# Performance work log

Hardware: AMD Instinct MI355X
Metric: run time of the kernel (lower is better)

The kernel has to match this reference:

```python
import jax, jax.numpy as jnp
import numpy as np

TW = 25; HID = 128; LAYERS = 6; SPATIAL = 1; NVAR = 1
TMAX = 4.0; TMIN = 0.0; RES_T = 250.0; DOM = 16.0
N = 65536; B = 8; E = 393216
EPS = 1e-5


def swish(x):
    return x * jax.nn.sigmoid(x)


def _forward(u, x_pos, t_pos, variables,
             emb_w1, emb_b1, emb_w2, emb_b2,
             m1_w, m1_b, m2_w, m2_b,
             u1_w, u1_b, u2_w, u2_b,
             c1_w, c1_b, c2_w, c2_b,
             edge_index, batch):
    t_norm = t_pos / TMAX                       # [N]
    pos = x_pos / DOM                           # [N, 1] normalized by domain extent
    node_in = jnp.concatenate([u, pos, t_norm[:, None], variables], axis=-1)
    f = swish(node_in @ emb_w1 + emb_b1)
    f = swish(f @ emb_w2 + emb_b2)              # [N, HID]

    var_all = jnp.concatenate([t_norm[:, None], variables], axis=-1)  # [N, NVAR+1]
    src, dst = edge_index[0], edge_index[1]     # PyG: x_j = x[src], x_i = x[dst]
    du = u[dst] - u[src]                        # [E, TW]
    dp = pos[dst] - pos[src]                    # [E, SPATIAL]
    v_i = var_all[dst]                          # [E, NVAR+1]

    ones_e = jnp.ones((E,), f.dtype)
    deg = jnp.maximum(jax.ops.segment_sum(ones_e, dst, num_segments=N), 1.0)
    ones_n = jnp.ones((N,), f.dtype)
    gcount = jnp.maximum(jax.ops.segment_sum(ones_n, batch, num_segments=B), 1.0)

    for l in range(LAYERS):
        # message: concat(x_i, x_j, u_i-u_j, pos_i-pos_j, vars_i) -> 2-layer MLP
        m = jnp.concatenate([f[dst], f[src], du, dp, v_i], axis=-1)  # [E, 284]
        m = swish(m @ m1_w[l] + m1_b[l])
        m = swish(m @ m2_w[l] + m2_b[l])
        agg = jax.ops.segment_sum(m, dst, num_segments=N) / deg[:, None]  # mean aggr
        # update: concat(x, message, vars) -> 2-layer MLP, residual (in==out)
        h = jnp.concatenate([f, agg, var_all], axis=-1)  # [N, 258]
        h = swish(h @ u1_w[l] + u1_b[l])
        h = swish(h @ u2_w[l] + u2_b[l])
        h = f + h
        # InstanceNorm over nodes within each graph, per feature (no affine)
        mean = jax.ops.segment_sum(h, batch, num_segments=B) / gcount[:, None]
        var = jax.ops.segment_sum(h * h, batch, num_segments=B) / gcount[:, None] - mean * mean
        f = (h - mean[batch]) * jax.lax.rsqrt(var[batch] + EPS)

    # output CNN head over feature axis: [N, 1, HID] -> [N, 1, TW]
    y = jax.lax.conv_general_dilated(f[:, None, :], c1_w, (3,), 'VALID',
                                     dimension_numbers=('NCH', 'OIH', 'NCH'))
    y = swish(y + c1_b[None, :, None])
    y = jax.lax.conv_general_dilated(y, c2_w, (1,), 'VALID',
                                     dimension_numbers=('NCH', 'OIH', 'NCH'))
    diff = y[:, 0, :] + c2_b[0]                 # [N, TW]

    dt = jnp.cumsum(jnp.full((TW,), (TMAX - TMIN) / RES_T, dtype=f.dtype))
    out = u[:, -1][:, None] + dt[None, :] * diff
    return out


def setup_inputs() -> dict:
    key = jax.random.key(0)
    keys = iter(jax.random.split(key, 128))

    def lin(i, o):
        s = 1.0 / np.sqrt(i)
        w = jax.random.uniform(next(keys), (i, o), jnp.float32, -s, s)
        b = jax.random.uniform(next(keys), (o,), jnp.float32, -s, s)
        return w, b

    def stacked(i, o):
        ws, bs = zip(*[lin(i, o) for _ in range(LAYERS)])
        return jnp.stack(ws), jnp.stack(bs)

    def conv(o, i, k):
        s = 1.0 / np.sqrt(i * k)
        w = jax.random.uniform(next(keys), (o, i, k), jnp.float32, -s, s)
        b = jax.random.uniform(next(keys), (o,), jnp.float32, -s, s)
        return w, b

    emb_w1, emb_b1 = lin(TW + SPATIAL + 1 + NVAR, HID)
    emb_w2, emb_b2 = lin(HID, HID)
    m1_w, m1_b = stacked(2 * HID + TW + SPATIAL + NVAR + 1, HID)
    m2_w, m2_b = stacked(HID, HID)
    u1_w, u1_b = stacked(2 * HID + NVAR + 1, HID)
    u2_w, u2_b = stacked(HID, HID)
    c1_w, c1_b = conv(8, 1, 16)
    c2_w, c2_b = conv(1, 8, 14)

    u = jax.random.normal(next(keys), (N, TW), jnp.float32)
    x_pos = jax.random.uniform(next(keys), (N, SPATIAL), jnp.float32) * DOM
    t_pos = jax.random.uniform(next(keys), (N,), jnp.float32) * TMAX
    variables = jax.random.normal(next(keys), (N, NVAR), jnp.float32)
    edge_index = jax.random.randint(next(keys), (2, E), 0, N, jnp.int32)
    batch = jnp.sort(jax.random.randint(next(keys), (N,), 0, B, jnp.int32))

    return {'u': u, 'x_pos': x_pos, 't_pos': t_pos, 'variables': variables,
            'edge_index': edge_index, 'batch': batch,
            'emb_w1': emb_w1, 'emb_b1': emb_b1, 'emb_w2': emb_w2, 'emb_b2': emb_b2,
            'm1_w': m1_w, 'm1_b': m1_b, 'm2_w': m2_w, 'm2_b': m2_b,
            'u1_w': u1_w, 'u1_b': u1_b, 'u2_w': u2_w, 'u2_b': u2_b,
            'c1_w': c1_w, 'c1_b': c1_b, 'c2_w': c2_w, 'c2_b': c2_b}


def reference(u, x_pos, t_pos, variables, edge_index, batch,
              emb_w1, emb_b1, emb_w2, emb_b2,
              m1_w, m1_b, m2_w, m2_b,
              u1_w, u1_b, u2_w, u2_b,
              c1_w, c1_b, c2_w, c2_b):
    return _forward(u, x_pos, t_pos, variables,
                    emb_w1, emb_b1, emb_w2, emb_b2,
                    m1_w, m1_b, m2_w, m2_b,
                    u1_w, u1_b, u2_w, u2_b,
                    c1_w, c1_b, c2_w, c2_b,
                    edge_index, batch)
```

## Files before the change

### kernel.cpp

```cpp
#include <hip/hip_runtime.h>
#include <hip/hip_bf16.h>

#define N_NODES 65536
#define N_EDGES 393216
#define NB 8
#define HID 128
#define TW 25
#define LAYERS 6
#define BGRAPH 8
#define EPSF 1e-5f
#define TILE_E 128

typedef __attribute__((ext_vector_type(8))) short bf16x8;
typedef __attribute__((ext_vector_type(4))) float f32x4;

__device__ __forceinline__ float swishf(float x) {
    float den = 1.0f + __expf(-x);
    float r;
    asm("v_rcp_f32 %0, %1" : "=v"(r) : "v"(den));
    return x * r;
}

__device__ __forceinline__ unsigned short f2bf(float x) {
    unsigned int u = __float_as_uint(x);
    u += 0x7fffu + ((u >> 16) & 1u);
    return (unsigned short)(u >> 16);
}

__device__ __forceinline__ unsigned int cvtpk2bf(float lo, float hi) {
    unsigned int r;
    asm("v_cvt_pk_bf16_f32 %0, %1, %2" : "=v"(r) : "v"(lo), "v"(hi));
    return r;
}

__device__ __forceinline__ unsigned short f2bf_rne(float x) {
    unsigned int r;
    asm("v_cvt_pk_bf16_f32 %0, %1, %2" : "=v"(r) : "v"(x), "v"(x));
    return (unsigned short)r;
}

__device__ __forceinline__ float bf2f(unsigned short v) {
    return __uint_as_float(((unsigned int)v) << 16);
}

__global__ void gcount_kernel(const int* __restrict__ batch, float* __restrict__ gcount) {
    int b = threadIdx.x;
    if (b >= BGRAPH) return;
    auto lb = [&](int key) {
        int lo = 0, hi = N_NODES;
        while (lo < hi) { int mid = (lo + hi) >> 1; if (batch[mid] < key) lo = mid + 1; else hi = mid; }
        return lo;
    };
    int c = lb(b + 1) - lb(b);
    gcount[b] = c > 0 ? (float)c : 1.0f;
}

__global__ void count_kernel(const int* __restrict__ ei, int* __restrict__ cnt) {
    int e = blockIdx.x * 256 + threadIdx.x;
    if (e < N_EDGES) atomicAdd(&cnt[ei[N_EDGES + e]], 1);
}

__global__ __launch_bounds__(256) void block_sum_kernel(const int* __restrict__ cnt, int* __restrict__ bsum) {
    __shared__ int s[256];
    int t = threadIdx.x;
    s[t] = cnt[blockIdx.x * 256 + t];
    __syncthreads();
    for (int st = 128; st > 0; st >>= 1) {
        if (t < st) s[t] += s[t + st];
        __syncthreads();
    }
    if (t == 0) bsum[blockIdx.x] = s[0];
}

__global__ __launch_bounds__(256) void scan_bsum_kernel(const int* __restrict__ bsum, int* __restrict__ bpref) {
    __shared__ int s[256];
    int t = threadIdx.x;
    int orig = bsum[t];
    s[t] = orig;
    __syncthreads();
    for (int st = 1; st < 256; st <<= 1) {
        int v = (t >= st) ? s[t - st] : 0;
        __syncthreads();
        s[t] += v;
        __syncthreads();
    }
    bpref[t] = s[t] - orig;
}

__global__ __launch_bounds__(256) void offsets_kernel(const int* __restrict__ cnt, const int* __restrict__ bpref,
                                                      int* __restrict__ cursor) {
    __shared__ int s[256];
    int t = threadIdx.x;
    int base = blockIdx.x * 256;
    int orig = cnt[base + t];
    s[t] = orig;
    __syncthreads();
    for (int st = 1; st < 256; st <<= 1) {
        int v = (t >= st) ? s[t - st] : 0;
        __syncthreads();
        s[t] += v;
        __syncthreads();
    }
    cursor[base + t] = s[t] - orig + bpref[blockIdx.x];
}

__global__ void scatter_kernel(const int* __restrict__ ei, int* __restrict__ cursor,
                               int* __restrict__ src_s, int* __restrict__ dst_s) {
    int e = blockIdx.x * 256 + threadIdx.x;
    if (e >= N_EDGES) return;
    int d = ei[N_EDGES + e];
    int pos = atomicAdd(&cursor[d], 1);
    src_s[pos] = ei[e];
    dst_s[pos] = d;
}

__global__ void w2bf_kernel(const float* __restrict__ m2_w, unsigned short* __restrict__ W2T) {
    int idx = blockIdx.x * 256 + threadIdx.x;
    int l = idx >> 14;
    int rem = idx & 16383;
    int n = rem >> 7, k = rem & 127;
    W2T[idx] = f2bf(m2_w[l * 16384 + k * HID + n]);
}

__global__ void w1t_kernel(const float* __restrict__ m1_w, unsigned short* __restrict__ wAB) {
    int idx = blockIdx.x * 256 + threadIdx.x;
    int l = idx / (2 * 128 * 160);
    int rem = idx % (2 * 128 * 160);
    int pass = rem / (128 * 160);
    int o = (rem % (128 * 160)) / 160;
    int k = rem % 160;
    const float* M = m1_w + (size_t)l * 284 * 128;
    float v;
    if (k < 128) {
        v = M[(pass ? 128 + k : k) * 128 + o];
    } else {
        int ku = k - 128;
        if (ku < 25) v = M[(256 + ku) * 128 + o];
        else if (ku == 25) v = M[281 * 128 + o];
        else if (ku == 26) v = M[282 * 128 + o];
        else if (ku == 27) v = M[283 * 128 + o];
        else v = 0.0f;
        if (pass) v = (ku <= 25) ? -v : 0.0f;
    }
    wAB[idx] = f2bf(v);
}

__global__ void u1t_kernel(const float* __restrict__ u1_w, unsigned short* __restrict__ U1T) {
    int idx = blockIdx.x * 256 + threadIdx.x;
    int l = idx >> 15;
    int o = (idx >> 8) & 127;
    int k = idx & 255;
    U1T[idx] = f2bf(u1_w[(size_t)l * 258 * 128 + k * 128 + o]);
}

__global__ void u2t_kernel(const float* __restrict__ u2_w, unsigned short* __restrict__ U2T) {
    int idx = blockIdx.x * 256 + threadIdx.x;
    int l = idx >> 14;
    int o = (idx >> 7) & 127;
    int k = idx & 127;
    U2T[idx] = f2bf(u2_w[(size_t)l * 16384 + k * 128 + o]);
}

__global__ void wemb_kernel(const float* __restrict__ ew1, const float* __restrict__ ew2,
                            unsigned short* __restrict__ we1T, unsigned short* __restrict__ we2T) {
    int idx = blockIdx.x * 256 + threadIdx.x;
    if (idx < 4096) {
        int o = idx >> 5, k = idx & 31;
        we1T[idx] = f2bf(k < 28 ? ew1[k * HID + o] : 0.0f);
    } else {
        int j = idx - 4096;
        int o = j >> 7, k = j & 127;
        we2T[j] = f2bf(ew2[k * HID + o]);
    }
}

__global__ void xin_kernel(const float* __restrict__ u, const float* __restrict__ xpos,
                           const float* __restrict__ tpos, const float* __restrict__ vars,
                           unsigned short* __restrict__ xin) {
    int idx = blockIdx.x * 256 + threadIdx.x;
    int n = idx >> 5, k = idx & 31;
    float v;
    if (k < 25) v = u[n * TW + k];
    else if (k == 25) v = xpos[n] * (1.0f / 16.0f);
    else if (k == 26) v = tpos[n] * 0.25f;
    else if (k == 27) v = vars[n];
    else v = 0.0f;
    xin[idx] = f2bf(v);
}

__device__ __forceinline__ void abv_chunk(
    const bf16x8 (&afr)[2][5], int nb, int lr, int lk, int colbase,
    const unsigned short* __restrict__ Wp, const float* __restrict__ b1,
    unsigned short* __restrict__ Op)
{
    f32x4 acc[2][2];
    #pragma unroll
    for (int rt = 0; rt < 2; ++rt)
        #pragma unroll
        for (int cf2 = 0; cf2 < 2; ++cf2)
            acc[rt][cf2] = (f32x4){0.0f, 0.0f, 0.0f, 0.0f};
    #pragma unroll
    for (int cf2 = 0; cf2 < 2; ++cf2) {
        const unsigned short* wrow = Wp + (colbase + cf2 * 16 + lr) * 160 + lk * 8;
        #pragma unroll
        for (int ks = 0; ks < 5; ++ks) {
            bf16x8 bfr = *reinterpret_cast<const bf16x8*>(wrow + ks * 32);
            acc[0][cf2] = __builtin_amdgcn_mfma_f32_16x16x32_bf16(afr[0][ks], bfr, acc[0][cf2], 0, 0, 0);
            acc[1][cf2] = __builtin_amdgcn_mfma_f32_16x16x32_bf16(afr[1][ks], bfr, acc[1][cf2], 0, 0, 0);
        }
    }
    #pragma unroll
    for (int cf2 = 0; cf2 < 2; ++cf2) {
        int col = colbase + cf2 * 16 + lr;
        float bb = b1 ? b1[col] : 0.0f;
        #pragma unroll
        for (int rt = 0; rt < 2; ++rt) {
            #pragma unroll
            for (int j = 0; j < 4; ++j) {
                int row = nb + rt * 16 + lk * 4 + j;
                Op[(size_t)row * HID + col] = f2bf_rne(acc[rt][cf2][j] + bb);
            }
        }
    }
}

__global__ __launch_bounds__(256) void emb_abv_kernel(
    const unsigned short* __restrict__ xin_bf,
    const unsigned short* __restrict__ we1T, const float* __restrict__ eb1,
    const unsigned short* __restrict__ we2T, const float* __restrict__ eb2,
    const unsigned short* __restrict__ wA, const unsigned short* __restrict__ wB,
    const float* __restrict__ b1,
    unsigned short* __restrict__ f_bf,
    unsigned short* __restrict__ A_bf, unsigned short* __restrict__ Bv_bf)
{
    __shared__ unsigned short q_lds[4 * 32 * HID];
    const int tid = threadIdx.x;
    const int w = tid >> 6, l = tid & 63;
    const int lr = l & 15, lk = l >> 4;
    const int nb = blockIdx.x * 128 + w * 32;
    char* qbase = reinterpret_cast<char*>(q_lds) + w * 8192;

    bf16x8 xfr[2];
    #pragma unroll
    for (int rt = 0; rt < 2; ++rt)
        xfr[rt] = *reinterpret_cast<const bf16x8*>(xin_bf + (size_t)(nb + rt * 16 + lr) * 32 + lk * 8);

    #pragma unroll 1
    for (int cc = 0; cc < 4; ++cc) {
        f32x4 acc1[2][2];
        #pragma unroll
        for (int rt = 0; rt < 2; ++rt)
            #pragma unroll
            for (int cf2 = 0; cf2 < 2; ++cf2)
                acc1[rt][cf2] = (f32x4){0.0f, 0.0f, 0.0f, 0.0f};
        #pragma unroll
        for (int cf2 = 0; cf2 < 2; ++cf2) {
            bf16x8 bfr = *reinterpret_cast<const bf16x8*>(we1T + ((cc * 2 + cf2) * 16 + lr) * 32 + lk * 8);
            acc1[0][cf2] = __builtin_amdgcn_mfma_f32_16x16x32_bf16(xfr[0], bfr, acc1[0][cf2], 0, 0, 0);
            acc1[1][cf2] = __builtin_amdgcn_mfma_f32_16x16x32_bf16(xfr[1], bfr, acc1[1][cf2], 0, 0, 0);
        }
        #pragma unroll
        for (int cf2 = 0; cf2 < 2; ++cf2) {
            int col = (cc * 2 + cf2) * 16 + lr;
            float bb = eb1[col];
            #pragma unroll
            for (int rt = 0; rt < 2; ++rt)
                #pragma unroll
                for (int j = 0; j < 4; ++j) {
                    float qv = swishf(acc1[rt][cf2][j] + bb);
                    int rloc = rt * 16 + lk * 4 + j;
                    *reinterpret_cast<unsigned short*>(qbase + rloc * 256 + ((col * 2) ^ ((rloc & 7) << 4))) = f2bf_rne(qv);
                }
        }
    }

    __shared__ unsigned short f_lds2[4 * 32 * HID];
    char* fbase = reinterpret_cast<char*>(f_lds2) + w * 8192;
    #pragma unroll 1
    for (int cc = 0; cc < 4; ++cc) {
        f32x4 acc2[2][2];
        #pragma unroll
        for (int rt = 0; rt < 2; ++rt)
            #pragma unroll
            for (int cf2 = 0; cf2 < 2; ++cf2)
                acc2[rt][cf2] = (f32x4){0.0f, 0.0f, 0.0f, 0.0f};
        #pragma unroll
        for (int ks = 0; ks < 4; ++ks) {
            bf16x8 afrq[2];
            #pragma unroll
            for (int rt = 0; rt < 2; ++rt) {
                int rloc = rt * 16 + lr;
                afrq[rt] = *reinterpret_cast<const bf16x8*>(qbase + rloc * 256 + ((ks * 64 + lk * 16) ^ ((rloc & 7) << 4)));
            }
            #pragma unroll
            for (int cf2 = 0; cf2 < 2; ++cf2) {
                bf16x8 bfr = *reinterpret_cast<const bf16x8*>(we2T + ((cc * 2 + cf2) * 16 + lr) * HID + ks * 32 + lk * 8);
                acc2[0][cf2] = __builtin_amdgcn_mfma_f32_16x16x32_bf16(afrq[0], bfr, acc2[0][cf2], 0, 0, 0);
                acc2[1][cf2] = __builtin_amdgcn_mfma_f32_16x16x32_bf16(afrq[1], bfr, acc2[1][cf2], 0, 0, 0);
            }
        }
        #pragma unroll
        for (int cf2 = 0; cf2 < 2; ++cf2) {
            int col = (cc * 2 + cf2) * 16 + lr;
            float bb = eb2[col];
            #pragma unroll
            for (int rt = 0; rt < 2; ++rt)
                #pragma unroll
                for (int j = 0; j < 4; ++j) {
                    float fv = swishf(acc2[rt][cf2][j] + bb);
                    unsigned short fb = f2bf_rne(fv);
                    int rloc = rt * 16 + lk * 4 + j;
                    f_bf[(size_t)(nb + rloc) * HID + col] = fb;
                    *reinterpret_cast<unsigned short*>(fbase + rloc * 256 + ((col * 2) ^ ((rloc & 7) << 4))) = fb;
                }
        }
    }

    bf16x8 afr[2][5];
    #pragma unroll
    for (int rt = 0; rt < 2; ++rt) {
        int rloc = rt * 16 + lr;
        #pragma unroll
        for (int ks = 0; ks < 4; ++ks)
            afr[rt][ks] = *reinterpret_cast<const bf16x8*>(fbase + rloc * 256 + ((ks * 64 + lk * 16) ^ ((rloc & 7) << 4)));
        afr[rt][4] = xfr[rt];
    }
    #pragma unroll 1
    for (int cc = 0; cc < 4; ++cc) abv_chunk(afr, nb, lr, lk, cc * 32, wA, b1, A_bf);
    #pragma unroll 1
    for (int cc = 0; cc < 4; ++cc) abv_chunk(afr, nb, lr, lk, cc * 32, wB, nullptr, Bv_bf);
}

__global__ __launch_bounds__(256) void norm_abv_kernel(
    const unsigned short* __restrict__ h, const int* __restrict__ batch,
    const float* __restrict__ dsum, const float* __restrict__ dsq,
    const float* __restrict__ gcount,
    const unsigned short* __restrict__ xin_bf,
    const unsigned short* __restrict__ wA, const unsigned short* __restrict__ wB,
    const float* __restrict__ b1,
    unsigned short* __restrict__ f_bf,
    unsigned short* __restrict__ A_bf, unsigned short* __restrict__ Bv_bf)
{
    __shared__ unsigned short f_lds[32 * HID];
    const int tid = threadIdx.x;
    const int w = tid >> 6, l = tid & 63;
    const int lr = l & 15, lk = l >> 4;
    const int nb = blockIdx.x * 32;

    {
        const int ks = w;
        const int c0 = ks * 32 + lk * 8;
        #pragma unroll
        for (int rt = 0; rt < 2; ++rt) {
            int row = nb + rt * 16 + lr;
            int b = batch[row];
            float inv = 1.0f / gcount[b];
            uint4 hv4 = *reinterpret_cast<const uint4*>(h + (size_t)row * HID + c0);
            unsigned int hw[4] = {hv4.x, hv4.y, hv4.z, hv4.w};
            float4 s0 = *reinterpret_cast<const float4*>(dsum + b * HID + c0);
            float4 s1 = *reinterpret_cast<const float4*>(dsum + b * HID + c0 + 4);
            float4 q0 = *reinterpret_cast<const float4*>(dsq + b * HID + c0);
            float4 q1 = *reinterpret_cast<const float4*>(dsq + b * HID + c0 + 4);
            float o[8];
            #pragma unroll
            for (int i = 0; i < 8; ++i) {
                float hx = (i & 1) ? __uint_as_float(hw[i >> 1] & 0xffff0000u)
                                   : __uint_as_float(hw[i >> 1] << 16);
                float sm = (i < 4) ? reinterpret_cast<const float*>(&s0)[i] : reinterpret_cast<const float*>(&s1)[i - 4];
                float sq = (i < 4) ? reinterpret_cast<const float*>(&q0)[i] : reinterpret_cast<const float*>(&q1)[i - 4];
                float mean = sm * inv;
                float var = sq * inv - mean * mean;
                o[i] = (hx - mean) * rsqrtf(var + EPSF);
            }
            uint4 t;
            t.x = cvtpk2bf(o[0], o[1]);
            t.y = cvtpk2bf(o[2], o[3]);
            t.z = cvtpk2bf(o[4], o[5]);
            t.w = cvtpk2bf(o[6], o[7]);
            *reinterpret_cast<uint4*>(f_bf + (size_t)row * HID + c0) = t;
            int rloc = rt * 16 + lr;
            *reinterpret_cast<uint4*>(reinterpret_cast<char*>(f_lds) + rloc * 256 + ((c0 * 2) ^ ((rloc & 7) << 4))) = t;
        }
    }
    __syncthreads();

    bf16x8 afr[2][5];
    #pragma unroll
    for (int rt = 0; rt < 2; ++rt) {
        int rloc = rt * 16 + lr;
        #pragma unroll
        for (int ks = 0; ks < 4; ++ks)
            afr[rt][ks] = *reinterpret_cast<const bf16x8*>(
                reinterpret_cast<const char*>(f_lds) + rloc * 256 + ((ks * 64 + lk * 16) ^ ((rloc & 7) << 4)));
        afr[rt][4] = *reinterpret_cast<const bf16x8*>(xin_bf + (size_t)(nb + rt * 16 + lr) * 32 + lk * 8);
    }
    abv_chunk(afr, nb, lr, lk, w * 32, wA, b1, A_bf);
    abv_chunk(afr, nb, lr, lk, w * 32, wB, nullptr, Bv_bf);
}

__global__ __launch_bounds__(256) void edge_mfma_kernel(
    const int* __restrict__ src_s, const int* __restrict__ dst_s,
    const unsigned short* __restrict__ A_bf, const unsigned short* __restrict__ Bv_bf,
    const unsigned short* __restrict__ W2T, const float* __restrict__ b2,
    float* __restrict__ agg)
{
    const int tid = threadIdx.x;
    const int w = tid >> 6, l = tid & 63;
    const int lr = l & 15, lk = l >> 4;
    const int e0 = blockIdx.x * TILE_E + w * 32;

    bf16x8 afr[2][4];
    #pragma unroll
    for (int rt = 0; rt < 2; ++rt) {
        int e = e0 + ((lr >> 2) << 3) + rt * 4 + (lr & 3);
        int dn = dst_s[e], sn = src_s[e];
        const unsigned short* ap = A_bf + (size_t)dn * HID + lk * 8;
        const unsigned short* bp = Bv_bf + (size_t)sn * HID + lk * 8;
        #pragma unroll
        for (int ks = 0; ks < 4; ++ks) {
            uint4 av = *reinterpret_cast<const uint4*>(ap + ks * 32);
            uint4 bv = *reinterpret_cast<const uint4*>(bp + ks * 32);
            auto proc = [](unsigned int aw, unsigned int bw) -> unsigned int {
                float a0 = __uint_as_float(aw << 16), a1 = __uint_as_float(aw & 0xffff0000u);
                float b0 = __uint_as_float(bw << 16), b1 = __uint_as_float(bw & 0xffff0000u);
                return cvtpk2bf(swishf(a0 + b0), swishf(a1 + b1));
            };
            union { bf16x8 v; unsigned int u[4]; } t;
            t.u[0] = proc(av.x, bv.x);
            t.u[1] = proc(av.y, bv.y);
            t.u[2] = proc(av.z, bv.z);
            t.u[3] = proc(av.w, bv.w);
            afr[rt][ks] = t.v;
        }
    }

    const int ebase = e0 + lk * 8;
    int4 dA4 = *reinterpret_cast<const int4*>(dst_s + ebase);
    int4 dB4 = *reinterpret_cast<const int4*>(dst_s + ebase + 4);
    int d[8] = {dA4.x, dA4.y, dA4.z, dA4.w, dB4.x, dB4.y, dB4.z, dB4.w};
    bool sm[7];
    int roff[8];
    #pragma unroll
    for (int m = 0; m < 7; ++m) sm[m] = (d[m + 1] == d[m]);
    #pragma unroll
    for (int m = 0; m < 8; ++m) roff[m] = d[m] * HID;

    #pragma unroll 1
    for (int cc = 0; cc < 4; ++cc) {
        f32x4 acc[2][2];
        #pragma unroll
        for (int rt = 0; rt < 2; ++rt)
            #pragma unroll
            for (int cf2 = 0; cf2 < 2; ++cf2)
                acc[rt][cf2] = (f32x4){0.0f, 0.0f, 0.0f, 0.0f};
        #pragma unroll
        for (int cf2 = 0; cf2 < 2; ++cf2) {
            const unsigned short* wrow = W2T + ((cc * 2 + cf2) * 16 + lr) * HID + lk * 8;
            #pragma unroll
            for (int ks = 0; ks < 4; ++ks) {
                bf16x8 bfr = *reinterpret_cast<const bf16x8*>(wrow + ks * 32);
                acc[0][cf2] = __builtin_amdgcn_mfma_f32_16x16x32_bf16(afr[0][ks], bfr, acc[0][cf2], 0, 0, 0);
                acc[1][cf2] = __builtin_amdgcn_mfma_f32_16x16x32_bf16(afr[1][ks], bfr, acc[1][cf2], 0, 0, 0);
            }
        }
        #pragma unroll
        for (int cf2 = 0; cf2 < 2; ++cf2) {
            int col = (cc * 2 + cf2) * 16 + lr;
            float bias = b2[col];
            float v[8];
            #pragma unroll
            for (int m = 0; m < 8; ++m) v[m] = swishf(acc[m >> 2][cf2][m & 3] + bias);
            float run = v[0];
            #pragma unroll
            for (int m = 1; m < 8; ++m) {
                if (sm[m - 1]) run += v[m];
                else { atomicAdd(&agg[(size_t)roff[m - 1] + col], run); run = v[m]; }
            }
            atomicAdd(&agg[(size_t)roff[7] + col], run);
        }
    }
}

__global__ __launch_bounds__(256) void update_mfma_kernel(
    const unsigned short* __restrict__ f_bf, const float* __restrict__ agg,
    const int* __restrict__ cnt,
    const float* __restrict__ tpos, const float* __restrict__ vars,
    const int* __restrict__ batch,
    const unsigned short* __restrict__ U1T, const float* __restrict__ u1tv,
    const float* __restrict__ b1, const unsigned short* __restrict__ U2T,
    const float* __restrict__ b2, unsigned short* __restrict__ h,
    float* __restrict__ dsum, float* __restrict__ dsq)
{
    __shared__ unsigned short q_lds[32 * HID];
    const int tid = threadIdx.x;
    const int w = tid >> 6, l = tid & 63;
    const int lr = l & 15, lk = l >> 4;
    const int nb = blockIdx.x * 32;

    float invd[2];
    #pragma unroll
    for (int rt = 0; rt < 2; ++rt) {
        int c = cnt[nb + rt * 16 + lr];
        invd[rt] = 1.0f / (float)(c > 0 ? c : 1);
    }
    float tn[2][4], vn[2][4];
    #pragma unroll
    for (int rt = 0; rt < 2; ++rt)
        #pragma unroll
        for (int j = 0; j < 4; ++j) {
            int row = nb + rt * 16 + lk * 4 + j;
            tn[rt][j] = tpos[row] * 0.25f;
            vn[rt][j] = vars[row];
        }

    {
        f32x4 acc[2][2];
        #pragma unroll
        for (int rt = 0; rt < 2; ++rt)
            #pragma unroll
            for (int cf2 = 0; cf2 < 2; ++cf2)
                acc[rt][cf2] = (f32x4){0.0f, 0.0f, 0.0f, 0.0f};
        #pragma unroll
        for (int ks = 0; ks < 8; ++ks) {
            bf16x8 afr[2];
            #pragma unroll
            for (int rt = 0; rt < 2; ++rt) {
                int row = nb + rt * 16 + lr;
                if (ks < 4) {
                    afr[rt] = *reinterpret_cast<const bf16x8*>(f_bf + (size_t)row * HID + ks * 32 + lk * 8);
                } else {
                    const float* ap = agg + (size_t)row * HID + (ks - 4) * 32 + lk * 8;
                    float4 a0 = *reinterpret_cast<const float4*>(ap);
                    float4 a1 = *reinterpret_cast<const float4*>(ap + 4);
                    float iv = invd[rt];
                    union { bf16x8 v; unsigned int u[4]; } t;
                    t.u[0] = cvtpk2bf(a0.x * iv, a0.y * iv);
                    t.u[1] = cvtpk2bf(a0.z * iv, a0.w * iv);
                    t.u[2] = cvtpk2bf(a1.x * iv, a1.y * iv);
                    t.u[3] = cvtpk2bf(a1.z * iv, a1.w * iv);
                    afr[rt] = t.v;
                }
            }
            #pragma unroll
            for (int cf2 = 0; cf2 < 2; ++cf2) {
                bf16x8 bfr = *reinterpret_cast<const bf16x8*>(U1T + ((w * 2 + cf2) * 16 + lr) * 256 + ks * 32 + lk * 8);
                acc[0][cf2] = __builtin_amdgcn_mfma_f32_16x16x32_bf16(afr[0], bfr, acc[0][cf2], 0, 0, 0);
                acc[1][cf2] = __builtin_amdgcn_mfma_f32_16x16x32_bf16(afr[1], bfr, acc[1][cf2], 0, 0, 0);
            }
        }
        #pragma unroll
        for (int cf2 = 0; cf2 < 2; ++cf2) {
            int col = w * 32 + cf2 * 16 + lr;
            float bb = b1[col], wt = u1tv[col], wv = u1tv[HID + col];
            #pragma unroll
            for (int rt = 0; rt < 2; ++rt)
                #pragma unroll
                for (int j = 0; j < 4; ++j) {
                    float qv = swishf(acc[rt][cf2][j] + bb + tn[rt][j] * wt + vn[rt][j] * wv);
                    int rloc = rt * 16 + lk * 4 + j;
                    *reinterpret_cast<unsigned short*>(reinterpret_cast<char*>(q_lds) + rloc * 256 + ((col * 2) ^ ((rloc & 7) << 4))) = f2bf_rne(qv);
                }
        }
    }
    __syncthreads();

    const int bfirst = batch[nb];
    const bool uni = (bfirst == batch[nb + 31]);
    {
        f32x4 acc2[2][2];
        #pragma unroll
        for (int rt = 0; rt < 2; ++rt)
            #pragma unroll
            for (int cf2 = 0; cf2 < 2; ++cf2)
                acc2[rt][cf2] = (f32x4){0.0f, 0.0f, 0.0f, 0.0f};
        #pragma unroll
        for (int ks = 0; ks < 4; ++ks) {
            bf16x8 afr[2];
            #pragma unroll
            for (int rt = 0; rt < 2; ++rt) {
                int rloc = rt * 16 + lr;
                afr[rt] = *reinterpret_cast<const bf16x8*>(
                    reinterpret_cast<const char*>(q_lds) + rloc * 256 + ((ks * 64 + lk * 16) ^ ((rloc & 7) << 4)));
            }
            #pragma unroll
            for (int cf2 = 0; cf2 < 2; ++cf2) {
                bf16x8 bfr = *reinterpret_cast<const bf16x8*>(U2T + ((w * 2 + cf2) * 16 + lr) * HID + ks * 32 + lk * 8);
                acc2[0][cf2] = __builtin_amdgcn_mfma_f32_16x16x32_bf16(afr[0], bfr, acc2[0][cf2], 0, 0, 0);
                acc2[1][cf2] = __builtin_amdgcn_mfma_f32_16x16x32_bf16(afr[1], bfr, acc2[1][cf2], 0, 0, 0);
            }
        }
        #pragma unroll
        for (int cf2 = 0; cf2 < 2; ++cf2) {
            int col = w * 32 + cf2 * 16 + lr;
            float bb = b2[col];
            float s = 0.0f, s2 = 0.0f;
            #pragma unroll
            for (int rt = 0; rt < 2; ++rt)
                #pragma unroll
                for (int j = 0; j < 4; ++j) {
                    int row = nb + rt * 16 + lk * 4 + j;
                    float fres = bf2f(f_bf[(size_t)row * HID + col]);
                    float hv = fres + swishf(acc2[rt][cf2][j] + bb);
                    unsigned short hb = f2bf_rne(hv);
                    h[(size_t)row * HID + col] = hb;
                    float hvr = bf2f(hb);
                    if (uni) { s += hvr; s2 += hvr * hvr; }
                    else {
                        int b = batch[row];
                        atomicAdd(&dsum[b * HID + col], hvr);
                        atomicAdd(&dsq[b * HID + col], hvr * hvr);
                    }
                }
            if (uni) {
                s += __shfl_xor(s, 16); s += __shfl_xor(s, 32);
                s2 += __shfl_xor(s2, 16); s2 += __shfl_xor(s2, 32);
                if (lk == 0) {
                    atomicAdd(&dsum[bfirst * HID + col], s);
                    atomicAdd(&dsq[bfirst * HID + col], s2);
                }
            }
        }
    }
}

__global__ __launch_bounds__(256) void head_kernel(
    const unsigned short* __restrict__ h, const int* __restrict__ batch,
    const float* __restrict__ dsum, const float* __restrict__ dsq,
    const float* __restrict__ gcount,
    const float* __restrict__ u,
    const float* __restrict__ c1w, const float* __restrict__ c1b,
    const float* __restrict__ c2w, const float* __restrict__ c2b,
    float* __restrict__ out)
{
    __shared__ float fs[16][HID];
    __shared__ float y1[16][8][40];
    const int tid = threadIdx.x;
    const int n0 = blockIdx.x * 16;
    {
        int node = tid >> 4, cb = tid & 15;
        int n = n0 + node;
        int b = batch[n];
        float inv = 1.0f / gcount[b];
        int c0 = cb * 8;
        uint4 v = *reinterpret_cast<const uint4*>(h + (size_t)n * HID + c0);
        unsigned int wv[4] = {v.x, v.y, v.z, v.w};
        #pragma unroll
        for (int i = 0; i < 8; ++i) {
            float hx = (i & 1) ? __uint_as_float(wv[i >> 1] & 0xffff0000u)
                               : __uint_as_float(wv[i >> 1] << 16);
            float mean = dsum[b * HID + c0 + i] * inv;
            float var = dsq[b * HID + c0 + i] * inv - mean * mean;
            fs[node][c0 + i] = (hx - mean) * rsqrtf(var + EPSF);
        }
    }
    __syncthreads();
    {
        const int node = tid >> 4;
        const int rem = tid & 15;
        const int o = rem >> 1;
        const int ph = rem & 1;
        const float cb = c1b[o];
        float wk[16];
        #pragma unroll
        for (int k = 0; k < 16; ++k) wk[k] = c1w[o * 16 + k];
        for (int p = ph * 19; p < ph * 19 + 19; ++p) {
            float acc = cb;
            #pragma unroll
            for (int k = 0; k < 16; ++k) acc += fs[node][p * 3 + k] * wk[k];
            y1[node][o][p] = swishf(acc);
        }
    }
    __syncthreads();
    const float cb2 = c2b[0];
    #pragma unroll
    for (int pass = 0; pass < 2; ++pass) {
        int unit = tid + pass * 256;
        if (unit < 16 * TW) {
            int node = unit / TW, t = unit % TW;
            float acc = cb2;
            #pragma unroll
            for (int o = 0; o < 8; ++o)
                #pragma unroll
                for (int k = 0; k < 14; ++k)
                    acc += y1[node][o][t + k] * c2w[o * 14 + k];
            int n = n0 + node;
            out[n * TW + t] = u[n * TW + (TW - 1)] + (0.016f * (float)(t + 1)) * acc;
        }
    }
}

extern "C" void kernel_launch(void* const* d_in, const int* in_sizes, int n_in,
                              void* d_out, int out_size, void* d_ws, size_t ws_size,
                              hipStream_t stream)
{
    (void)in_sizes; (void)n_in; (void)out_size; (void)ws_size;
    const float* u      = (const float*)d_in[0];
    const float* xpos   = (const float*)d_in[1];
    const float* tpos   = (const float*)d_in[2];
    const float* vars   = (const float*)d_in[3];
    const int*   ei     = (const int*)d_in[4];
    const int*   batch  = (const int*)d_in[5];
    const float* emb_w1 = (const float*)d_in[6];
    const float* emb_b1 = (const float*)d_in[7];
    const float* emb_w2 = (const float*)d_in[8];
    const float* emb_b2 = (const float*)d_in[9];
    const float* m1_w   = (const float*)d_in[10];
    const float* m1_b   = (const float*)d_in[11];
    const float* m2_w   = (const float*)d_in[12];
    const float* m2_b   = (const float*)d_in[13];
    const float* u1_w   = (const float*)d_in[14];
    const float* u1_b   = (const float*)d_in[15];
    const float* u2_w   = (const float*)d_in[16];
    const float* u2_b   = (const float*)d_in[17];
    const float* c1w    = (const float*)d_in[18];
    const float* c1b    = (const float*)d_in[19];
    const float* c2w    = (const float*)d_in[20];
    const float* c2b    = (const float*)d_in[21];
    float* out = (float*)d_out;

    char* ws = (char*)d_ws;
    const size_t fbytes = (size_t)N_NODES * HID * sizeof(float);
    float* agg    = (float*)(ws);
    char*  p      = ws + fbytes;
    unsigned short* h_bf   = (unsigned short*)p;  p += (size_t)N_NODES * HID * 2;
    unsigned short* A_bf   = (unsigned short*)p;  p += (size_t)N_NODES * HID * 2;
    unsigned short* Bv_bf  = (unsigned short*)p;  p += (size_t)N_NODES * HID * 2;
    unsigned short* f_bf   = (unsigned short*)p;  p += (size_t)N_NODES * HID * 2;
    unsigned short* xin_bf = (unsigned short*)p;  p += (size_t)N_NODES * 32 * 2;
    int* cnt      = (int*)p;               p += (size_t)N_NODES * 4;
    int* cursor   = (int*)p;               p += (size_t)N_NODES * 4;
    int* src_s    = (int*)p;               p += (size_t)N_EDGES * 4;
    int* dst_s    = (int*)p;               p += (size_t)N_EDGES * 4;
    int* bsum     = (int*)p;               p += 256 * 4;
    int* bpref    = (int*)p;               p += 256 * 4;
    float* dsumL  = (float*)p;             p += (size_t)LAYERS * BGRAPH * HID * 4;
    float* dsqL   = (float*)p;             p += (size_t)LAYERS * BGRAPH * HID * 4;
    float* gcount = (float*)p;             p += BGRAPH * 4;
    unsigned short* W2T  = (unsigned short*)p;  p += (size_t)LAYERS * HID * HID * 2;
    unsigned short* wAB  = (unsigned short*)p;  p += (size_t)LAYERS * 2 * 128 * 160 * 2;
    unsigned short* U1T  = (unsigned short*)p;  p += (size_t)LAYERS * 128 * 256 * 2;
    unsigned short* U2T  = (unsigned short*)p;  p += (size_t)LAYERS * 128 * 128 * 2;
    unsigned short* we1T = (unsigned short*)p;  p += 128 * 32 * 2;
    unsigned short* we2T = (unsigned short*)p;  p += 128 * 128 * 2;

    hipMemsetAsync(cnt, 0, (size_t)N_NODES * 4, stream);
    count_kernel<<<N_EDGES / 256, 256, 0, stream>>>(ei, cnt);
    block_sum_kernel<<<N_NODES / 256, 256, 0, stream>>>(cnt, bsum);
    scan_bsum_kernel<<<1, 256, 0, stream>>>(bsum, bpref);
    offsets_kernel<<<N_NODES / 256, 256, 0, stream>>>(cnt, bpref, cursor);
    scatter_kernel<<<N_EDGES / 256, 256, 0, stream>>>(ei, cursor, src_s, dst_s);

    w2bf_kernel<<<LAYERS * HID * HID / 256, 256, 0, stream>>>(m2_w, W2T);
    w1t_kernel<<<LAYERS * 2 * 128 * 160 / 256, 256, 0, stream>>>(m1_w, wAB);
    u1t_kernel<<<LAYERS * 128 * 256 / 256, 256, 0, stream>>>(u1_w, U1T);
    u2t_kernel<<<LAYERS * 128 * 128 / 256, 256, 0, stream>>>(u2_w, U2T);
    wemb_kernel<<<80, 256, 0, stream>>>(emb_w1, emb_w2, we1T, we2T);
    xin_kernel<<<N_NODES * 32 / 256, 256, 0, stream>>>(u, xpos, tpos, vars, xin_bf);
    gcount_kernel<<<1, 64, 0, stream>>>(batch, gcount);
    hipMemsetAsync(dsumL, 0, (size_t)2 * LAYERS * BGRAPH * HID * 4, stream);

    emb_abv_kernel<<<N_NODES / 128, 256, 0, stream>>>(
        xin_bf, we1T, emb_b1, we2T, emb_b2,
        wAB, wAB + 128 * 160, m1_b, f_bf, A_bf, Bv_bf);

    for (int l = 0; l < LAYERS; ++l) {
        hipMemsetAsync(agg, 0, fbytes, stream);
        edge_mfma_kernel<<<N_EDGES / TILE_E, 256, 0, stream>>>(
            src_s, dst_s, A_bf, Bv_bf, W2T + (size_t)l * HID * HID,
            m2_b + (size_t)l * HID, agg);
        update_mfma_kernel<<<N_NODES / 32, 256, 0, stream>>>(
            f_bf, agg, cnt, tpos, vars, batch,
            U1T + (size_t)l * 128 * 256,
            u1_w + (size_t)l * 258 * 128 + 256 * 128,
            u1_b + (size_t)l * HID,
            U2T + (size_t)l * 128 * 128,
            u2_b + (size_t)l * HID, h_bf,
            dsumL + (size_t)l * BGRAPH * HID, dsqL + (size_t)l * BGRAPH * HID);
        if (l < LAYERS - 1) {
            norm_abv_kernel<<<N_NODES / 32, 256, 0, stream>>>(
                h_bf, batch, dsumL + (size_t)l * BGRAPH * HID, dsqL + (size_t)l * BGRAPH * HID,
                gcount, xin_bf,
                wAB + (size_t)(l + 1) * 2 * 128 * 160,
                wAB + (size_t)(l + 1) * 2 * 128 * 160 + 128 * 160,
                m1_b + (size_t)(l + 1) * HID,
                f_bf, A_bf, Bv_bf);
        }
    }
    head_kernel<<<N_NODES / 16, 256, 0, stream>>>(
        h_bf, batch, dsumL + (size_t)(LAYERS - 1) * BGRAPH * HID,
        dsqL + (size_t)(LAYERS - 1) * BGRAPH * HID, gcount,
        u, c1w, c1b, c2w, c2b, out);
}
```

Baseline: 1.180 ms.

## Accumulate edge aggregation in bf16 via packed atomics and fuse zeroing into update

```diff
diff --git a/kernel.cpp b/kernel.cpp
--- a/kernel.cpp
+++ b/kernel.cpp
@@ -41,6 +41,10 @@
 
 __device__ __forceinline__ float bf2f(unsigned short v) {
     return __uint_as_float(((unsigned int)v) << 16);
+}
+
+__device__ __forceinline__ void atomic_pk_bf16(unsigned short* addr, unsigned int data) {
+    asm volatile("global_atomic_pk_add_bf16 %0, %1, off" :: "v"(addr), "v"(data) : "memory");
 }
 
 __global__ void gcount_kernel(const int* __restrict__ batch, float* __restrict__ gcount) {
@@ -112,6 +116,12 @@
     int pos = atomicAdd(&cursor[d], 1);
     src_s[pos] = ei[e];
     dst_s[pos] = d;
+}
+
+__global__ void invdeg_kernel(const int* __restrict__ cnt, float* __restrict__ inv_deg) {
+    int n = blockIdx.x * 256 + threadIdx.x;
+    int c = cnt[n];
+    inv_deg[n] = 1.0f / (float)(c > 0 ? c : 1);
 }
 
 __global__ void w2bf_kernel(const float* __restrict__ m2_w, unsigned short* __restrict__ W2T) {
@@ -400,9 +410,10 @@
 
 __global__ __launch_bounds__(256) void edge_mfma_kernel(
     const int* __restrict__ src_s, const int* __restrict__ dst_s,
+    const float* __restrict__ inv_deg,
     const unsigned short* __restrict__ A_bf, const unsigned short* __restrict__ Bv_bf,
     const unsigned short* __restrict__ W2T, const float* __restrict__ b2,
-    float* __restrict__ agg)
+    unsigned short* __restrict__ agg_bf)
 {
     const int tid = threadIdx.x;
     const int w = tid >> 6, l = tid & 63;
@@ -440,10 +451,13 @@
     int d[8] = {dA4.x, dA4.y, dA4.z, dA4.w, dB4.x, dB4.y, dB4.z, dB4.w};
     bool sm[7];
     int roff[8];
+    float ivd8[8];
     #pragma unroll
     for (int m = 0; m < 7; ++m) sm[m] = (d[m + 1] == d[m]);
     #pragma unroll
     for (int m = 0; m < 8; ++m) roff[m] = d[m] * HID;
+    #pragma unroll
+    for (int m = 0; m < 8; ++m) ivd8[m] = inv_deg[d[m]];
 
     #pragma unroll 1
     for (int cc = 0; cc < 4; ++cc) {
@@ -467,6 +481,8 @@
         for (int cf2 = 0; cf2 < 2; ++cf2) {
             int col = (cc * 2 + cf2) * 16 + lr;
             float bias = b2[col];
+            int colb = col & ~1;
+            bool hi = (col & 1) != 0;
             float v[8];
             #pragma unroll
             for (int m = 0; m < 8; ++m) v[m] = swishf(acc[m >> 2][cf2][m & 3] + bias);
@@ -474,16 +490,22 @@
             #pragma unroll
             for (int m = 1; m < 8; ++m) {
                 if (sm[m - 1]) run += v[m];
-                else { atomicAdd(&agg[(size_t)roff[m - 1] + col], run); run = v[m]; }
-            }
-            atomicAdd(&agg[(size_t)roff[7] + col], run);
+                else {
+                    float x = run * ivd8[m - 1];
+                    unsigned int pk = cvtpk2bf(hi ? 0.0f : x, hi ? x : 0.0f);
+                    atomic_pk_bf16(agg_bf + (size_t)roff[m - 1] + colb, pk);
+                    run = v[m];
+                }
+            }
+            float x = run * ivd8[7];
+            unsigned int pk = cvtpk2bf(hi ? 0.0f : x, hi ? x : 0.0f);
+            atomic_pk_bf16(agg_bf + (size_t)roff[7] + colb, pk);
         }
     }
 }
 
 __global__ __launch_bounds__(256) void update_mfma_kernel(
-    const unsigned short* __restrict__ f_bf, const float* __restrict__ agg,
-    const int* __restrict__ cnt,
+    const unsigned short* __restrict__ f_bf, unsigned short* __restrict__ agg_bf,
     const float* __restrict__ tpos, const float* __restrict__ vars,
     const int* __restrict__ batch,
     const unsigned short* __restrict__ U1T, const float* __restrict__ u1tv,
@@ -497,12 +519,6 @@
     const int lr = l & 15, lk = l >> 4;
     const int nb = blockIdx.x * 32;
 
-    float invd[2];
-    #pragma unroll
-    for (int rt = 0; rt < 2; ++rt) {
-        int c = cnt[nb + rt * 16 + lr];
-        invd[rt] = 1.0f / (float)(c > 0 ? c : 1);
-    }
     float tn[2][4], vn[2][4];
     #pragma unroll
     for (int rt = 0; rt < 2; ++rt)
@@ -526,20 +542,8 @@
             #pragma unroll
             for (int rt = 0; rt < 2; ++rt) {
                 int row = nb + rt * 16 + lr;
-                if (ks < 4) {
-                    afr[rt] = *reinterpret_cast<const bf16x8*>(f_bf + (size_t)row * HID + ks * 32 + lk * 8);
-                } else {
-                    const float* ap = agg + (size_t)row * HID + (ks - 4) * 32 + lk * 8;
-                    float4 a0 = *reinterpret_cast<const float4*>(ap);
-                    float4 a1 = *reinterpret_cast<const float4*>(ap + 4);
-                    float iv = invd[rt];
-                    union { bf16x8 v; unsigned int u[4]; } t;
-                    t.u[0] = cvtpk2bf(a0.x * iv, a0.y * iv);
-                    t.u[1] = cvtpk2bf(a0.z * iv, a0.w * iv);
-                    t.u[2] = cvtpk2bf(a1.x * iv, a1.y * iv);
-                    t.u[3] = cvtpk2bf(a1.z * iv, a1.w * iv);
-                    afr[rt] = t.v;
-                }
+                const unsigned short* base = (ks < 4) ? f_bf : agg_bf;
+                afr[rt] = *reinterpret_cast<const bf16x8*>(base + (size_t)row * HID + (ks & 3) * 32 + lk * 8);
             }
             #pragma unroll
             for (int cf2 = 0; cf2 < 2; ++cf2) {
@@ -563,6 +567,16 @@
         }
     }
     __syncthreads();
+
+    {
+        uint4 z = {0u, 0u, 0u, 0u};
+        #pragma unroll
+        for (int i = 0; i < 2; ++i) {
+            int q = tid + i * 256;
+            int r = q >> 4, cb = q & 15;
+            *reinterpret_cast<uint4*>(agg_bf + (size_t)(nb + r) * HID + cb * 8) = z;
+        }
+    }
 
     const int bfirst = batch[nb];
     const bool uni = (bfirst == batch[nb + 31]);
@@ -719,9 +733,8 @@
     float* out = (float*)d_out;
 
     char* ws = (char*)d_ws;
-    const size_t fbytes = (size_t)N_NODES * HID * sizeof(float);
-    float* agg    = (float*)(ws);
-    char*  p      = ws + fbytes;
+    char*  p      = ws;
+    unsigned short* agg_bf = (unsigned short*)p;  p += (size_t)N_NODES * HID * 2;
     unsigned short* h_bf   = (unsigned short*)p;  p += (size_t)N_NODES * HID * 2;
     unsigned short* A_bf   = (unsigned short*)p;  p += (size_t)N_NODES * HID * 2;
     unsigned short* Bv_bf  = (unsigned short*)p;  p += (size_t)N_NODES * HID * 2;
@@ -729,6 +742,7 @@
     unsigned short* xin_bf = (unsigned short*)p;  p += (size_t)N_NODES * 32 * 2;
     int* cnt      = (int*)p;               p += (size_t)N_NODES * 4;
     int* cursor   = (int*)p;               p += (size_t)N_NODES * 4;
+    float* inv_deg = (float*)p;            p += (size_t)N_NODES * 4;
     int* src_s    = (int*)p;               p += (size_t)N_EDGES * 4;
     int* dst_s    = (int*)p;               p += (size_t)N_EDGES * 4;
     int* bsum     = (int*)p;               p += 256 * 4;
@@ -749,6 +763,7 @@
     scan_bsum_kernel<<<1, 256, 0, stream>>>(bsum, bpref);
     offsets_kernel<<<N_NODES / 256, 256, 0, stream>>>(cnt, bpref, cursor);
     scatter_kernel<<<N_EDGES / 256, 256, 0, stream>>>(ei, cursor, src_s, dst_s);
+    invdeg_kernel<<<N_NODES / 256, 256, 0, stream>>>(cnt, inv_deg);
 
     w2bf_kernel<<<LAYERS * HID * HID / 256, 256, 0, stream>>>(m2_w, W2T);
     w1t_kernel<<<LAYERS * 2 * 128 * 160 / 256, 256, 0, stream>>>(m1_w, wAB);
@@ -758,18 +773,18 @@
     xin_kernel<<<N_NODES * 32 / 256, 256, 0, stream>>>(u, xpos, tpos, vars, xin_bf);
     gcount_kernel<<<1, 64, 0, stream>>>(batch, gcount);
     hipMemsetAsync(dsumL, 0, (size_t)2 * LAYERS * BGRAPH * HID * 4, stream);
+    hipMemsetAsync(agg_bf, 0, (size_t)N_NODES * HID * 2, stream);
 
     emb_abv_kernel<<<N_NODES / 128, 256, 0, stream>>>(
         xin_bf, we1T, emb_b1, we2T, emb_b2,
         wAB, wAB + 128 * 160, m1_b, f_bf, A_bf, Bv_bf);
 
     for (int l = 0; l < LAYERS; ++l) {
-        hipMemsetAsync(agg, 0, fbytes, stream);
         edge_mfma_kernel<<<N_EDGES / TILE_E, 256, 0, stream>>>(
-            src_s, dst_s, A_bf, Bv_bf, W2T + (size_t)l * HID * HID,
-            m2_b + (size_t)l * HID, agg);
+            src_s, dst_s, inv_deg, A_bf, Bv_bf, W2T + (size_t)l * HID * HID,
+            m2_b + (size_t)l * HID, agg_bf);
         update_mfma_kernel<<<N_NODES / 32, 256, 0, stream>>>(
-            f_bf, agg, cnt, tpos, vars, batch,
+            f_bf, agg_bf, tpos, vars, batch,
             U1T + (size_t)l * 128 * 256,
             u1_w + (size_t)l * 258 * 128 + 256 * 128,
             u1_b + (size_t)l * HID,
```

Result: slower. 2.019 ms (+71.1%).
